# Optimization experiments

Hardware: AMD Instinct MI355X
Metric: run time of the kernel (lower is better)

The kernel has to match this reference:

```python
import jax, jax.numpy as jnp
import numpy as np

B, N, NY = 2, 4096, 4096
ENC_DIM, DEC_DIM, H = 768, 512, 8
HEAD_DIM = DEC_DIM // H
SCALE = HEAD_DIM ** -0.5


def setup_inputs() -> dict:
    key = jax.random.key(0)
    ks = jax.random.split(key, 8)
    lim_q = 1.0 / np.sqrt(DEC_DIM)
    lim_kv = 1.0 / np.sqrt(ENC_DIM)
    return {
        "x": jax.random.normal(ks[0], (B, N, DEC_DIM), jnp.float32),
        "y": jax.random.normal(ks[1], (B, NY, ENC_DIM), jnp.float32),
        "key_padding_mask": jax.random.randint(ks[2], (B, NY), 0, 2).astype(bool),
        "Wq": jax.random.uniform(ks[3], (DEC_DIM, DEC_DIM), jnp.float32, -lim_q, lim_q),
        "Wkv": jax.random.uniform(ks[4], (2 * DEC_DIM, ENC_DIM), jnp.float32, -lim_kv, lim_kv),
        "Wp": jax.random.uniform(ks[5], (DEC_DIM, DEC_DIM), jnp.float32, -lim_q, lim_q),
        "bp": jax.random.uniform(ks[6], (DEC_DIM,), jnp.float32, -lim_q, lim_q),
    }


def reference(x, y, key_padding_mask, Wq, Wkv, Wp, bp):
    # q projection: [B,N,C] -> [B,H,N,D]
    q = (x @ Wq.T).reshape(B, N, H, HEAD_DIM).transpose(0, 2, 1, 3)
    # kv projection: [B,Ny,E] -> [B,Ny,2C] -> k,v each [B,H,Ny,D]
    kv = (y @ Wkv.T).reshape(B, NY, 2, H, HEAD_DIM).transpose(2, 0, 3, 1, 4)
    k, v = kv[0], kv[1]
    # attention scores [B,H,N,Ny]
    attn = jnp.einsum("bhnd,bhmd->bhnm", q, k) * SCALE
    attn = jnp.where(key_padding_mask[:, None, None, :], -jnp.inf, attn)
    attn = jax.nn.softmax(attn, axis=-1)
    out = jnp.einsum("bhnm,bhmd->bhnd", attn, v)  # [B,H,N,D]
    out = out.transpose(0, 2, 1, 3).reshape(B, N, DEC_DIM)
    return out @ Wp.T + bp
```

## Files before the change

kernel.cpp:

```cpp
#include <hip/hip_runtime.h>
#include <hip/hip_bf16.h>
#include <stdint.h>

typedef __bf16 bf16_t;
typedef __bf16 bf16x8 __attribute__((ext_vector_type(8)));
typedef __bf16 bf16x4 __attribute__((ext_vector_type(4)));
typedef float  f32x4  __attribute__((ext_vector_type(4)));

#define MFMA16(a, b, c) __builtin_amdgcn_mfma_f32_16x16x32_bf16((a), (b), (c), 0, 0, 0)

__device__ __forceinline__ void gload_lds16(const void* g, void* l) {
  __builtin_amdgcn_global_load_lds((const __attribute__((address_space(1))) void*)g,
                                   (__attribute__((address_space(3))) void*)l, 16, 0, 0);
}

#define QSCALE 0.18033688011112042f
#define NE_X   4194304UL
#define NE_Y   6291456UL
#define NE_WQ  262144UL
#define NE_WKV 786432UL
#define NE_WP  262144UL
#define NE_BP  512UL

__global__ void detect_and_mask(const uint16_t* __restrict__ xu,
                                const uint8_t* __restrict__ mk,
                                int* __restrict__ flags, bf16_t* __restrict__ mmul) {
  __shared__ int cbf, c3f1, c3f3, cnz;
  const int t = threadIdx.x;
  if (t == 0) { cbf = 0; c3f1 = 0; c3f3 = 0; cnz = 0; }
  __syncthreads();
  if (blockIdx.x == 0) {
    int local = 0;
    for (int i = t; i < 2048; i += 256) {
      uint16_t u = xu[2 * i];
      int e = (u >> 7) & 0xFF;
      if (u == 0 || (e >= 0x66 && e <= 0x88)) local++;
    }
    atomicAdd(&cbf, local);
  }
  int l1 = 0, l3 = 0, lnz = 0;
  for (int i = t; i < 4096; i += 256) {
    uint8_t b = mk[i];
    int p = i & 3;
    if (p == 1 && b == 0x3F) l1++;
    if (p == 3 && b == 0x3F) l3++;
    if (p != 0 && b != 0) lnz++;
  }
  atomicAdd(&c3f1, l1);
  atomicAdd(&c3f3, l3);
  atomicAdd(&cnz, lnz);
  __syncthreads();
  if (blockIdx.x == 0 && t == 0) flags[0] = (cbf > 1536) ? 1 : 0;
  const int fmt = (c3f1 > 0) ? 2 : (c3f3 > 0) ? 3 : (cnz > 0) ? 0 : 1;
  const int i = blockIdx.x * 256 + t;
  bool on;
  if (fmt == 0)      on = mk[i] != 0;
  else if (fmt == 1) on = ((const int*)mk)[i] != 0;
  else if (fmt == 2) on = (((const uint16_t*)mk)[i] & 0x7FFF) != 0;
  else               on = ((const float*)mk)[i] != 0.0f;
  mmul[i] = on ? (bf16_t)0.0f : (bf16_t)1.0f;
}

__global__ void convert_all(const void* __restrict__ x, const void* __restrict__ y,
                            const void* __restrict__ wq, const void* __restrict__ wkv,
                            const void* __restrict__ wp, const void* __restrict__ bp,
                            uint16_t* __restrict__ dst, const int* __restrict__ flags) {
  const size_t E0 = NE_X, E1 = E0 + NE_Y, E2 = E1 + NE_WQ, E3 = E2 + NE_WKV,
               E4 = E3 + NE_WP, E5 = E4 + NE_BP;
  size_t i8 = ((size_t)blockIdx.x * 256 + threadIdx.x) * 8;
  if (i8 >= E5) return;
  const void* src; size_t off;
  if      (i8 < E0) { src = x;   off = i8; }
  else if (i8 < E1) { src = y;   off = i8 - E0; }
  else if (i8 < E2) { src = wq;  off = i8 - E1; }
  else if (i8 < E3) { src = wkv; off = i8 - E2; }
  else if (i8 < E4) { src = wp;  off = i8 - E3; }
  else              { src = bp;  off = i8 - E4; }
  const bool isWq = (i8 >= E1 && i8 < E2);
  if (flags[0] && !isWq) {
    *(uint4*)(dst + i8) = *(const uint4*)((const uint16_t*)src + off);
    return;
  }
  float v[8];
  if (flags[0]) {
    const uint16_t* u = (const uint16_t*)src + off;
    for (int j = 0; j < 8; ++j) {
      union { uint32_t q; float f; } c; c.q = ((uint32_t)u[j]) << 16; v[j] = c.f;
    }
  } else {
    const float* f = (const float*)src + off;
    float4 a = *(const float4*)f;
    float4 b2 = *(const float4*)(f + 4);
    v[0] = a.x; v[1] = a.y; v[2] = a.z; v[3] = a.w;
    v[4] = b2.x; v[5] = b2.y; v[6] = b2.z; v[7] = b2.w;
  }
  const float sc = isWq ? QSCALE : 1.0f;
  union { bf16_t h[8]; uint4 u; } pk;
  for (int j = 0; j < 8; ++j) pk.h[j] = (bf16_t)(v[j] * sc);
  *(uint4*)(dst + i8) = pk.u;
}

template <int K, int MODE>
__launch_bounds__(256, 2)
__global__ void gemm_bt(const bf16_t* __restrict__ A, const bf16_t* __restrict__ W,
                        const bf16_t* __restrict__ bias, void* __restrict__ C,
                        bf16_t* __restrict__ Vt, const int* __restrict__ flags, int Ncols) {
  __shared__ __align__(16) char lds[16384];
  char* ldsA = lds;
  char* ldsW = lds + 8192;
  const int t = threadIdx.x;
  const int w = t >> 6, lane = t & 63, quad = lane >> 4, l16 = lane & 15;
  const int wr = w >> 1, wc = w & 1;
  const int m0 = blockIdx.y * 128, n0 = blockIdx.x * 128;

  f32x4 acc[4][4] = {};
  const int rowS = t >> 2, uS = t & 3;

  for (int k0 = 0; k0 < K; k0 += 32) {
    __syncthreads();
    for (int i = 0; i < 2; ++i) {
      int row = i * 64 + rowS;
      int c = uS ^ ((row >> 1) & 3);
      gload_lds16(A + (size_t)(m0 + row) * K + k0 + c * 8, ldsA + i * 4096 + w * 1024);
      gload_lds16(W + (size_t)(n0 + row) * K + k0 + c * 8, ldsW + i * 4096 + w * 1024);
    }
    __syncthreads();
    bf16x8 af[4], bfr[4];
    for (int mt = 0; mt < 4; ++mt) {
      int row = wr * 64 + mt * 16 + l16;
      int us = quad ^ ((row >> 1) & 3);
      af[mt] = *(const bf16x8*)(ldsA + row * 64 + us * 16);
    }
    for (int nt = 0; nt < 4; ++nt) {
      int row = wc * 64 + nt * 16 + l16;
      int us = quad ^ ((row >> 1) & 3);
      bfr[nt] = *(const bf16x8*)(ldsW + row * 64 + us * 16);
    }
    for (int mt = 0; mt < 4; ++mt)
      for (int nt = 0; nt < 4; ++nt)
        acc[mt][nt] = MFMA16(af[mt], bfr[nt], acc[mt][nt]);
  }

  const int mbase = m0 + wr * 64;
  for (int nt = 0; nt < 4; ++nt) {
    const int col = n0 + wc * 64 + nt * 16 + l16;
    if (MODE == 1 && col >= 512) {
      const int hd = col - 512;
      const int hh = hd >> 6, d = hd & 63;
      const int dt = d >> 4, l15 = d & 15;
      for (int mt = 0; mt < 4; ++mt) {
        int m = mbase + mt * 16 + quad * 4;
        int bb = m >> 12, keyg = m & 4095;
        int kt = keyg >> 6, keyin = keyg & 63;
        int kc = (keyin >> 5) & 1, jq = (keyin >> 3) & 3, j0 = keyin & 7;
        const bf16_t* mmp = bias + bb * 4096 + keyg;
        union { bf16_t h4[4]; uint2 u; } pk;
        for (int r = 0; r < 4; ++r) pk.h4[r] = (bf16_t)(acc[mt][nt][r] * (float)mmp[r]);
        size_t base = (((size_t)(bb * 8 + hh) * 64 + kt) * 8 + dt * 2 + kc) * 1024
                      + (jq * 16 + l15) * 16 + j0 * 2;
        *(uint2*)((char*)Vt + base) = pk.u;
      }
    } else if (MODE == 1) {
      for (int mt = 0; mt < 4; ++mt) {
        int m = mbase + mt * 16 + quad * 4;
        for (int r = 0; r < 4; ++r)
          ((bf16_t*)C)[(size_t)(m + r) * 512 + col] = (bf16_t)acc[mt][nt][r];
      }
    } else if (MODE == 0) {
      for (int mt = 0; mt < 4; ++mt) {
        int m = mbase + mt * 16 + quad * 4;
        for (int r = 0; r < 4; ++r)
          ((bf16_t*)C)[(size_t)(m + r) * Ncols + col] = (bf16_t)acc[mt][nt][r];
      }
    } else {
      const float bv = (float)bias[col];
      const bool obf = (flags[0] != 0);
      for (int mt = 0; mt < 4; ++mt) {
        int m = mbase + mt * 16 + quad * 4;
        for (int r = 0; r < 4; ++r) {
          float v = acc[mt][nt][r] + bv;
          if (obf) ((bf16_t*)C)[(size_t)(m + r) * Ncols + col] = (bf16_t)v;
          else     ((float*)C)[(size_t)(m + r) * Ncols + col] = v;
        }
      }
    }
  }
}

__launch_bounds__(256, 2)
__global__ void attn(const bf16_t* __restrict__ Qb, const bf16_t* __restrict__ Kb,
                     const bf16_t* __restrict__ Vfb, const bf16_t* __restrict__ mmul,
                     bf16_t* __restrict__ Ob) {
  const int t = threadIdx.x, w = t >> 6, lane = t & 63, quad = lane >> 4, l16 = lane & 15;
  const int q0 = blockIdx.x * 128, h = blockIdx.y, b = blockIdx.z;

  __shared__ __align__(16) char lds[32768];
  char* Pw = lds + 16384 + w * 4096;
  char* Qs = lds + 16384;

  for (int i = 0; i < 4; ++i) {
    int row = i * 32 + (t >> 3);
    int c = (t & 7) ^ (row & 7);
    gload_lds16(Qb + (size_t)(b * 4096 + q0 + row) * 512 + h * 64 + c * 8,
                Qs + i * 4096 + w * 1024);
  }
  for (int i = 0; i < 2; ++i) {
    int row = i * 32 + (t >> 3);
    int c = (t & 7) ^ (row & 7);
    gload_lds16(Kb + (size_t)(b * 4096 + row) * 512 + h * 64 + c * 8,
                lds + i * 4096 + w * 1024);
  }
  __syncthreads();

  bf16x8 qf[2][2];
  for (int ng = 0; ng < 2; ++ng)
    for (int kc = 0; kc < 2; ++kc) {
      int row = 32 * w + 16 * ng + l16;
      int u = (4 * kc + quad) ^ (row & 7);
      qf[ng][kc] = *(const bf16x8*)(Qs + row * 128 + u * 16);
    }
  __syncthreads();

  f32x4 o[2][4] = {};
  f32x4 lacc[2] = {};
  const char* Vfbase = (const char*)Vfb + (size_t)(b * 8 + h) * 524288;

  for (int kt = 0; kt < 64; ++kt) {
    const int cur = kt & 1;
    const int kt0 = kt * 64;
    if (kt + 1 < 64) {
      const int nxt = cur ^ 1;
      for (int i = 0; i < 2; ++i) {
        int row = i * 32 + (t >> 3);
        int c = (t & 7) ^ (row & 7);
        gload_lds16(Kb + (size_t)(b * 4096 + kt0 + 64 + row) * 512 + h * 64 + c * 8,
                    lds + nxt * 8192 + i * 4096 + w * 1024);
      }
    }
    const char* Kl = lds + cur * 8192;

    bf16x8 mf[2];
    mf[0] = *(const bf16x8*)(mmul + b * 4096 + kt0 + quad * 8);
    mf[1] = *(const bf16x8*)(mmul + b * 4096 + kt0 + 32 + quad * 8);
    const char* Vtile = Vfbase + (size_t)kt * 8192;
    bf16x8 vf[4][2];
    for (int dt = 0; dt < 4; ++dt)
      for (int kc = 0; kc < 2; ++kc)
        vf[dt][kc] = *(const bf16x8*)(Vtile + (dt * 2 + kc) * 1024 + lane * 16);

    bf16x8 kf[4][2];
    for (int mt = 0; mt < 4; ++mt)
      for (int kc = 0; kc < 2; ++kc) {
        int row = mt * 16 + l16;
        int u = (4 * kc + quad) ^ (row & 7);
        kf[mt][kc] = *(const bf16x8*)(Kl + row * 128 + u * 16);
      }

    for (int ng = 0; ng < 2; ++ng) {
      const int row = 16 * ng + l16;
      for (int mt = 0; mt < 4; ++mt) {
        f32x4 z = {};
        z = MFMA16(kf[mt][0], qf[ng][0], z);
        z = MFMA16(kf[mt][1], qf[ng][1], z);
        bf16x4 pk;
        pk.x = (bf16_t)__builtin_amdgcn_exp2f(z[0]);
        pk.y = (bf16_t)__builtin_amdgcn_exp2f(z[1]);
        pk.z = (bf16_t)__builtin_amdgcn_exp2f(z[2]);
        pk.w = (bf16_t)__builtin_amdgcn_exp2f(z[3]);
        int c2 = (2 * mt + (quad >> 1)) ^ (row & 7);
        *(bf16x4*)(Pw + row * 128 + c2 * 16 + (quad & 1) * 8) = pk;
      }
    }

    bf16x8 pf[2][2];
    for (int ng = 0; ng < 2; ++ng)
      for (int kc = 0; kc < 2; ++kc) {
        int row = 16 * ng + l16;
        int u = (4 * kc + quad) ^ (row & 7);
        pf[ng][kc] = *(const bf16x8*)(Pw + row * 128 + u * 16);
      }
    for (int ng = 0; ng < 2; ++ng) {
      lacc[ng] = MFMA16(pf[ng][0], mf[0], lacc[ng]);
      lacc[ng] = MFMA16(pf[ng][1], mf[1], lacc[ng]);
    }
    for (int dt = 0; dt < 4; ++dt)
      for (int kc = 0; kc < 2; ++kc) {
        o[0][dt] = MFMA16(pf[0][kc], vf[dt][kc], o[0][dt]);
        o[1][dt] = MFMA16(pf[1][kc], vf[dt][kc], o[1][dt]);
      }

    __syncthreads();
  }

  for (int ng = 0; ng < 2; ++ng) {
    float inv[4];
    for (int r = 0; r < 4; ++r) inv[r] = 1.0f / lacc[ng][r];
    for (int dt = 0; dt < 4; ++dt)
      for (int r = 0; r < 4; ++r) {
        int q = q0 + 32 * w + 16 * ng + quad * 4 + r;
        int col = h * 64 + dt * 16 + l16;
        Ob[(size_t)(b * 4096 + q) * 512 + col] = (bf16_t)(o[ng][dt][r] * inv[r]);
      }
  }
}

extern "C" void kernel_launch(void* const* d_in, const int* in_sizes, int n_in,
                              void* d_out, int out_size, void* d_ws, size_t ws_size,
                              hipStream_t stream) {
  const void* x   = d_in[0];
  const void* y   = d_in[1];
  const void* msk = d_in[2];
  const void* Wq  = d_in[3];
  const void* Wkv = d_in[4];
  const void* Wp  = d_in[5];
  const void* bp  = d_in[6];

  char* ws = (char*)d_ws;
  bf16_t* Xb   = (bf16_t*)(ws + 0);
  bf16_t* Yb   = (bf16_t*)(ws + 8388608);
  bf16_t* Wqb  = (bf16_t*)(ws + 20971520);
  bf16_t* Wkvb = (bf16_t*)(ws + 21495808);
  bf16_t* Wpb  = (bf16_t*)(ws + 23068672);
  bf16_t* bpb  = (bf16_t*)(ws + 23592960);
  bf16_t* mmul = (bf16_t*)(ws + 23593984);
  int*    flags = (int*)(ws + 23610368);
  bf16_t* Kbuf  = (bf16_t*)(ws + 25165824);
  bf16_t* Vfrag = (bf16_t*)(ws + 33554432);
  bf16_t* Qbuf  = (bf16_t*)(ws + 8388608);
  bf16_t* Obuf  = (bf16_t*)(ws + 0);

  hipLaunchKernelGGL(detect_and_mask, dim3(32), dim3(256), 0, stream,
                     (const uint16_t*)x, (const uint8_t*)msk, flags, mmul);
  hipLaunchKernelGGL(convert_all, dim3(5761), dim3(256), 0, stream,
                     x, y, Wq, Wkv, Wp, bp, (uint16_t*)ws, flags);
  hipLaunchKernelGGL((gemm_bt<768, 1>), dim3(8, 64), dim3(256), 0, stream,
                     Yb, Wkvb, mmul, (void*)Kbuf, Vfrag, flags, 1024);
  hipLaunchKernelGGL((gemm_bt<512, 0>), dim3(4, 64), dim3(256), 0, stream,
                     Xb, Wqb, (const bf16_t*)nullptr, (void*)Qbuf, (bf16_t*)nullptr, flags, 512);
  hipLaunchKernelGGL(attn, dim3(32, 8, 2), dim3(256), 0, stream,
                     Qbuf, Kbuf, Vfrag, mmul, Obuf);
  hipLaunchKernelGGL((gemm_bt<512, 2>), dim3(4, 64), dim3(256), 0, stream,
                     Obuf, Wpb, bpb, d_out, (bf16_t*)nullptr, flags, 512);
}
```

Measured before the change: 269.6 us.

## Halve attention and GEMM block tiles to raise block count and occupancy

The attention kernel now handles 64 queries per block instead of 128, with one 16-row group per wave. This doubles the grid to 1024 blocks and reduces registers and LDS per block, and launch bounds are raised to 4 blocks per CU. The Q and output-projection GEMMs gain a BN template parameter and use 128x64 tiles, doubling their block counts to give better CU coverage. In exchange, each K and V tile is loaded and reused across fewer queries, so K/V traffic per unit of work doubles and each wave gets less MFMA work to hide latency.

```diff
diff --git a/kernel.cpp b/kernel.cpp
--- a/kernel.cpp
+++ b/kernel.cpp
@@ -100,20 +100,22 @@
   *(uint4*)(dst + i8) = pk.u;
 }
 
-template <int K, int MODE>
+template <int K, int MODE, int BN>
 __launch_bounds__(256, 2)
 __global__ void gemm_bt(const bf16_t* __restrict__ A, const bf16_t* __restrict__ W,
                         const bf16_t* __restrict__ bias, void* __restrict__ C,
                         bf16_t* __restrict__ Vt, const int* __restrict__ flags, int Ncols) {
-  __shared__ __align__(16) char lds[16384];
+  constexpr int MT = (BN == 128) ? 4 : 2;
+  __shared__ __align__(16) char lds[8192 + BN * 64];
   char* ldsA = lds;
   char* ldsW = lds + 8192;
   const int t = threadIdx.x;
   const int w = t >> 6, lane = t & 63, quad = lane >> 4, l16 = lane & 15;
-  const int wr = w >> 1, wc = w & 1;
-  const int m0 = blockIdx.y * 128, n0 = blockIdx.x * 128;
-
-  f32x4 acc[4][4] = {};
+  const int wr = (BN == 128) ? (w >> 1) : w;
+  const int wc = (BN == 128) ? (w & 1) : 0;
+  const int m0 = blockIdx.y * 128, n0 = blockIdx.x * BN;
+
+  f32x4 acc[MT][4] = {};
   const int rowS = t >> 2, uS = t & 3;
 
   for (int k0 = 0; k0 < K; k0 += 32) {
@@ -122,12 +124,16 @@
       int row = i * 64 + rowS;
       int c = uS ^ ((row >> 1) & 3);
       gload_lds16(A + (size_t)(m0 + row) * K + k0 + c * 8, ldsA + i * 4096 + w * 1024);
+    }
+    for (int i = 0; i < BN / 64; ++i) {
+      int row = i * 64 + rowS;
+      int c = uS ^ ((row >> 1) & 3);
       gload_lds16(W + (size_t)(n0 + row) * K + k0 + c * 8, ldsW + i * 4096 + w * 1024);
     }
     __syncthreads();
-    bf16x8 af[4], bfr[4];
-    for (int mt = 0; mt < 4; ++mt) {
-      int row = wr * 64 + mt * 16 + l16;
+    bf16x8 af[MT], bfr[4];
+    for (int mt = 0; mt < MT; ++mt) {
+      int row = wr * (MT * 16) + mt * 16 + l16;
       int us = quad ^ ((row >> 1) & 3);
       af[mt] = *(const bf16x8*)(ldsA + row * 64 + us * 16);
     }
@@ -136,19 +142,19 @@
       int us = quad ^ ((row >> 1) & 3);
       bfr[nt] = *(const bf16x8*)(ldsW + row * 64 + us * 16);
     }
-    for (int mt = 0; mt < 4; ++mt)
+    for (int mt = 0; mt < MT; ++mt)
       for (int nt = 0; nt < 4; ++nt)
         acc[mt][nt] = MFMA16(af[mt], bfr[nt], acc[mt][nt]);
   }
 
-  const int mbase = m0 + wr * 64;
+  const int mbase = m0 + wr * (MT * 16);
   for (int nt = 0; nt < 4; ++nt) {
     const int col = n0 + wc * 64 + nt * 16 + l16;
     if (MODE == 1 && col >= 512) {
       const int hd = col - 512;
       const int hh = hd >> 6, d = hd & 63;
       const int dt = d >> 4, l15 = d & 15;
-      for (int mt = 0; mt < 4; ++mt) {
+      for (int mt = 0; mt < MT; ++mt) {
         int m = mbase + mt * 16 + quad * 4;
         int bb = m >> 12, keyg = m & 4095;
         int kt = keyg >> 6, keyin = keyg & 63;
@@ -161,13 +167,13 @@
         *(uint2*)((char*)Vt + base) = pk.u;
       }
     } else if (MODE == 1) {
-      for (int mt = 0; mt < 4; ++mt) {
+      for (int mt = 0; mt < MT; ++mt) {
         int m = mbase + mt * 16 + quad * 4;
         for (int r = 0; r < 4; ++r)
           ((bf16_t*)C)[(size_t)(m + r) * 512 + col] = (bf16_t)acc[mt][nt][r];
       }
     } else if (MODE == 0) {
-      for (int mt = 0; mt < 4; ++mt) {
+      for (int mt = 0; mt < MT; ++mt) {
         int m = mbase + mt * 16 + quad * 4;
         for (int r = 0; r < 4; ++r)
           ((bf16_t*)C)[(size_t)(m + r) * Ncols + col] = (bf16_t)acc[mt][nt][r];
@@ -175,7 +181,7 @@
     } else {
       const float bv = (float)bias[col];
       const bool obf = (flags[0] != 0);
-      for (int mt = 0; mt < 4; ++mt) {
+      for (int mt = 0; mt < MT; ++mt) {
         int m = mbase + mt * 16 + quad * 4;
         for (int r = 0; r < 4; ++r) {
           float v = acc[mt][nt][r] + bv;
@@ -187,42 +193,37 @@
   }
 }
 
-__launch_bounds__(256, 2)
+__launch_bounds__(256, 4)
 __global__ void attn(const bf16_t* __restrict__ Qb, const bf16_t* __restrict__ Kb,
                      const bf16_t* __restrict__ Vfb, const bf16_t* __restrict__ mmul,
                      bf16_t* __restrict__ Ob) {
   const int t = threadIdx.x, w = t >> 6, lane = t & 63, quad = lane >> 4, l16 = lane & 15;
-  const int q0 = blockIdx.x * 128, h = blockIdx.y, b = blockIdx.z;
-
-  __shared__ __align__(16) char lds[32768];
-  char* Pw = lds + 16384 + w * 4096;
+  const int q0 = blockIdx.x * 64, h = blockIdx.y, b = blockIdx.z;
+
+  __shared__ __align__(16) char lds[24576];
+  char* Pw = lds + 16384 + w * 2048;
   char* Qs = lds + 16384;
 
-  for (int i = 0; i < 4; ++i) {
+  for (int i = 0; i < 2; ++i) {
     int row = i * 32 + (t >> 3);
     int c = (t & 7) ^ (row & 7);
     gload_lds16(Qb + (size_t)(b * 4096 + q0 + row) * 512 + h * 64 + c * 8,
                 Qs + i * 4096 + w * 1024);
-  }
-  for (int i = 0; i < 2; ++i) {
-    int row = i * 32 + (t >> 3);
-    int c = (t & 7) ^ (row & 7);
     gload_lds16(Kb + (size_t)(b * 4096 + row) * 512 + h * 64 + c * 8,
                 lds + i * 4096 + w * 1024);
   }
   __syncthreads();
 
-  bf16x8 qf[2][2];
-  for (int ng = 0; ng < 2; ++ng)
-    for (int kc = 0; kc < 2; ++kc) {
-      int row = 32 * w + 16 * ng + l16;
-      int u = (4 * kc + quad) ^ (row & 7);
-      qf[ng][kc] = *(const bf16x8*)(Qs + row * 128 + u * 16);
-    }
+  bf16x8 qf[2];
+  for (int kc = 0; kc < 2; ++kc) {
+    int row = 16 * w + l16;
+    int u = (4 * kc + quad) ^ (row & 7);
+    qf[kc] = *(const bf16x8*)(Qs + row * 128 + u * 16);
+  }
   __syncthreads();
 
-  f32x4 o[2][4] = {};
-  f32x4 lacc[2] = {};
+  f32x4 o[4] = {};
+  f32x4 lacc = {};
   const char* Vfbase = (const char*)Vfb + (size_t)(b * 8 + h) * 524288;
 
   for (int kt = 0; kt < 64; ++kt) {
@@ -256,12 +257,12 @@
         kf[mt][kc] = *(const bf16x8*)(Kl + row * 128 + u * 16);
       }
 
-    for (int ng = 0; ng < 2; ++ng) {
-      const int row = 16 * ng + l16;
+    {
+      const int row = l16;
       for (int mt = 0; mt < 4; ++mt) {
         f32x4 z = {};
-        z = MFMA16(kf[mt][0], qf[ng][0], z);
-        z = MFMA16(kf[mt][1], qf[ng][1], z);
+        z = MFMA16(kf[mt][0], qf[0], z);
+        z = MFMA16(kf[mt][1], qf[1], z);
         bf16x4 pk;
         pk.x = (bf16_t)__builtin_amdgcn_exp2f(z[0]);
         pk.y = (bf16_t)__builtin_amdgcn_exp2f(z[1]);
@@ -272,36 +273,30 @@
       }
     }
 
-    bf16x8 pf[2][2];
-    for (int ng = 0; ng < 2; ++ng)
-      for (int kc = 0; kc < 2; ++kc) {
-        int row = 16 * ng + l16;
-        int u = (4 * kc + quad) ^ (row & 7);
-        pf[ng][kc] = *(const bf16x8*)(Pw + row * 128 + u * 16);
-      }
-    for (int ng = 0; ng < 2; ++ng) {
-      lacc[ng] = MFMA16(pf[ng][0], mf[0], lacc[ng]);
-      lacc[ng] = MFMA16(pf[ng][1], mf[1], lacc[ng]);
-    }
-    for (int dt = 0; dt < 4; ++dt)
-      for (int kc = 0; kc < 2; ++kc) {
-        o[0][dt] = MFMA16(pf[0][kc], vf[dt][kc], o[0][dt]);
-        o[1][dt] = MFMA16(pf[1][kc], vf[dt][kc], o[1][dt]);
-      }
+    bf16x8 pf[2];
+    for (int kc = 0; kc < 2; ++kc) {
+      int row = l16;
+      int u = (4 * kc + quad) ^ (row & 7);
+      pf[kc] = *(const bf16x8*)(Pw + row * 128 + u * 16);
+    }
+    lacc = MFMA16(pf[0], mf[0], lacc);
+    lacc = MFMA16(pf[1], mf[1], lacc);
+    for (int dt = 0; dt < 4; ++dt) {
+      o[dt] = MFMA16(pf[0], vf[dt][0], o[dt]);
+      o[dt] = MFMA16(pf[1], vf[dt][1], o[dt]);
+    }
 
     __syncthreads();
   }
 
-  for (int ng = 0; ng < 2; ++ng) {
-    float inv[4];
-    for (int r = 0; r < 4; ++r) inv[r] = 1.0f / lacc[ng][r];
-    for (int dt = 0; dt < 4; ++dt)
-      for (int r = 0; r < 4; ++r) {
-        int q = q0 + 32 * w + 16 * ng + quad * 4 + r;
-        int col = h * 64 + dt * 16 + l16;
-        Ob[(size_t)(b * 4096 + q) * 512 + col] = (bf16_t)(o[ng][dt][r] * inv[r]);
-      }
-  }
+  float inv[4];
+  for (int r = 0; r < 4; ++r) inv[r] = 1.0f / lacc[r];
+  for (int dt = 0; dt < 4; ++dt)
+    for (int r = 0; r < 4; ++r) {
+      int q = q0 + 16 * w + quad * 4 + r;
+      int col = h * 64 + dt * 16 + l16;
+      Ob[(size_t)(b * 4096 + q) * 512 + col] = (bf16_t)(o[dt][r] * inv[r]);
+    }
 }
 
 extern "C" void kernel_launch(void* const* d_in, const int* in_sizes, int n_in,
@@ -333,12 +328,12 @@
                      (const uint16_t*)x, (const uint8_t*)msk, flags, mmul);
   hipLaunchKernelGGL(convert_all, dim3(5761), dim3(256), 0, stream,
                      x, y, Wq, Wkv, Wp, bp, (uint16_t*)ws, flags);
-  hipLaunchKernelGGL((gemm_bt<768, 1>), dim3(8, 64), dim3(256), 0, stream,
+  hipLaunchKernelGGL((gemm_bt<768, 1, 128>), dim3(8, 64), dim3(256), 0, stream,
                      Yb, Wkvb, mmul, (void*)Kbuf, Vfrag, flags, 1024);
-  hipLaunchKernelGGL((gemm_bt<512, 0>), dim3(4, 64), dim3(256), 0, stream,
+  hipLaunchKernelGGL((gemm_bt<512, 0, 64>), dim3(8, 64), dim3(256), 0, stream,
                      Xb, Wqb, (const bf16_t*)nullptr, (void*)Qbuf, (bf16_t*)nullptr, flags, 512);
-  hipLaunchKernelGGL(attn, dim3(32, 8, 2), dim3(256), 0, stream,
+  hipLaunchKernelGGL(attn, dim3(64, 8, 2), dim3(256), 0, stream,
                      Qbuf, Kbuf, Vfrag, mmul, Obuf);
-  hipLaunchKernelGGL((gemm_bt<512, 2>), dim3(4, 64), dim3(256), 0, stream,
+  hipLaunchKernelGGL((gemm_bt<512, 2, 64>), dim3(8, 64), dim3(256), 0, stream,
                      Obuf, Wpb, bpb, d_out, (bf16_t*)nullptr, flags, 512);
 }
```

Result: slower. 289.8 us (+7.5%).
